# Kernel optimization log

Measured on AMD Instinct MI355X. Metric: run time of the kernel, lower is better.

Reference implementation:

```python
import jax, jax.numpy as jnp
import numpy as np
import math

B, S, D_MODEL = 2, 2048, 1024
H = 16
DK = D_MODEL // H          # 64, down-proj per-stream dim
NOPE, ROPE = 128, 64
D_HEAD = NOPE + ROPE       # 192 = d_latent // H
D_LATENT = H * D_HEAD      # 3072
ROT_DIM = 2 * ((ROPE // 2) // 2)  # rotary dim actually rotated = qk_rope_dim//2 = 32
EPS = 1e-6


def _rmsnorm(x, w):
    out = x * jax.lax.rsqrt(jnp.mean(x * x, axis=-1, keepdims=True) + EPS)
    return out * w


def _apply_rope(x):
    # x: [b, h, s, d]; rotate first ROT_DIM channels, interleaved pairing
    s = x.shape[-2]
    inv_freq = 1.0 / (10000.0 ** (jnp.arange(0, ROT_DIM, 2, dtype=jnp.float32) / ROT_DIM))
    freqs = jnp.arange(s, dtype=jnp.float32)[:, None] * inv_freq[None, :]  # [s, ROT_DIM//2]
    freqs = jnp.repeat(freqs, 2, axis=-1)  # [s, ROT_DIM], (f0,f0,f1,f1,...)
    cos, sin = jnp.cos(freqs), jnp.sin(freqs)
    xl, xr = x[..., :ROT_DIM], x[..., ROT_DIM:]
    x1, x2 = xl[..., 0::2], xl[..., 1::2]
    rot = jnp.stack([-x2, x1], axis=-1).reshape(xl.shape)
    xl = xl * cos + rot * sin
    return jnp.concatenate([xl, xr], axis=-1)


def setup_inputs() -> dict:
    key = jax.random.key(0)
    ks = jax.random.split(key, 5)
    sc = 0.02
    x = jax.random.normal(ks[0], (B, S, D_MODEL), jnp.float32)
    mask = jnp.broadcast_to(jnp.tril(jnp.ones((S, S), jnp.int32)), (B, S, S))
    w_down = jax.random.normal(ks[1], (D_MODEL, 3 * DK), jnp.float32) * sc
    rms_w = jnp.ones((3 * DK,), jnp.float32)
    w_up = jax.random.normal(ks[2], (3 * DK, 3 * D_LATENT), jnp.float32) * sc
    w_o = jax.random.normal(ks[3], (D_LATENT, D_MODEL), jnp.float32) * sc
    return {"x": x, "mask": mask, "w_down": w_down, "rms_w": rms_w, "w_up": w_up, "w_o": w_o}


def reference(x, mask, w_down, rms_w, w_up, w_o):
    h = x @ w_down                        # [b, s, 3*dk]
    h = _rmsnorm(h, rms_w)
    qkv = h @ w_up                        # [b, s, 3*d_latent]
    q, k, v = jnp.split(qkv, 3, axis=-1)  # each [b, s, d_latent]

    def to_heads(t):
        # einops '(d h)': d outer, h inner
        return t.reshape(B, S, D_HEAD, H).transpose(0, 3, 1, 2)  # [b, h, s, d]

    q, k, v = to_heads(q), to_heads(k), to_heads(v)
    q_nope, q_rope = q[..., :NOPE], q[..., NOPE:]
    k_nope, k_rope = k[..., :NOPE], k[..., NOPE:]
    q_rope = _apply_rope(q_rope)
    k_rope = _apply_rope(k_rope)

    scores = (jnp.einsum('bhid,bhjd->bhij', q_nope, k_nope)
              + jnp.einsum('bhid,bhjd->bhij', q_rope, k_rope))
    scores = scores / math.sqrt(NOPE + ROPE)
    scores = jnp.where(mask[:, None] == 0, -1e9, scores)
    attn = jax.nn.softmax(scores, axis=-1)

    out = jnp.einsum('bhij,bhjd->bhid', attn, v)        # [b, h, s, d]
    out = out.transpose(0, 2, 1, 3).reshape(B, S, D_LATENT)  # 'b h s d -> b s (h d)'
    return out @ w_o
```

## Files before the change

### kernel.cpp

```cpp
#include <hip/hip_runtime.h>
#include <stdint.h>
#include <stddef.h>


typedef __bf16 bf16x8 __attribute__((ext_vector_type(8)));
typedef float  f32x4  __attribute__((ext_vector_type(4)));

#define MFMA16x16(a,b,c) __builtin_amdgcn_mfma_f32_16x16x32_bf16((a),(b),(c),0,0,0)

__device__ __forceinline__ uint16_t f2bf(float f){
  union { float f; uint32_t u; } v; v.f = f;
  uint32_t u = v.u + 0x7fffu + ((v.u >> 16) & 1u);
  return (uint16_t)(u >> 16);
}
__device__ __forceinline__ bf16x8 load_frag(const uint16_t* p){
  uint4 u = *reinterpret_cast<const uint4*>(p);
  return __builtin_bit_cast(bf16x8, u);
}
__device__ __forceinline__ f32x4 fzero(){
  f32x4 z = {0.f, 0.f, 0.f, 0.f};
  return z;
}
__device__ __forceinline__ uint32_t pack2(float a, float b){
  return (uint32_t)f2bf(a) | ((uint32_t)f2bf(b) << 16);
}
__device__ __forceinline__ void gl2lds16(const uint16_t* g, uint16_t* l){
  __builtin_amdgcn_global_load_lds(
      (const __attribute__((address_space(1))) uint32_t*)g,
      (__attribute__((address_space(3))) uint32_t*)l,
      16, 0, 0);
}

__global__ __launch_bounds__(256) void k_transpose_all(const float* __restrict__ w_up,
                                                       const float* __restrict__ w_o,
                                                       const float* __restrict__ w_down,
                                                       uint16_t* __restrict__ w_up_t,
                                                       uint16_t* __restrict__ w_o_t,
                                                       uint16_t* __restrict__ w_dn_t){
  __shared__ float t[32][33];
  int id = blockIdx.x;
  const float* in; uint16_t* out; int R, C, bx, by;
  if(id < 1728){ in = w_up;  out = w_up_t; R = 192;  C = 9216; bx = id % 288; by = id / 288; }
  else if(id < 4800){ id -= 1728; in = w_o; out = w_o_t; R = 3072; C = 1024; bx = id % 32; by = id / 32; }
  else { id -= 4800; in = w_down; out = w_dn_t; R = 1024; C = 192; bx = id % 6; by = id / 6; }
  const int tc = bx * 32, tr = by * 32;
  const int j = threadIdx.x & 31, i0 = threadIdx.x >> 5;
  for(int ii = 0; ii < 4; ++ii){
    int r = i0 + ii * 8;
    t[r][j] = in[(size_t)(tr + r) * C + tc + j];
  }
  __syncthreads();
  for(int ii = 0; ii < 4; ++ii){
    int c = i0 + ii * 8;
    out[(size_t)(tc + c) * R + tr + j] = f2bf(t[j][c]);
  }
}

__global__ __launch_bounds__(256) void k_down_mfma(const float* __restrict__ x,
                                                   const uint16_t* __restrict__ wdt,
                                                   const float* __restrict__ rms_w,
                                                   uint16_t* __restrict__ h_out){
  __shared__ __align__(16) uint16_t as[32 * 64];
  __shared__ float hsq[32];
  const int tid  = threadIdx.x;
  const int wave = tid >> 6, lane = tid & 63;
  const int ml = lane & 15, qd = lane >> 4;
  const int m0 = blockIdx.x * 32;
  const int n0w = wave * 48;
  if(tid < 32) hsq[tid] = 0.f;

  f32x4 acc[2][3];
#pragma unroll
  for(int mt = 0; mt < 2; ++mt)
#pragma unroll
    for(int nt = 0; nt < 3; ++nt) acc[mt][nt] = fzero();

  const int srow = tid >> 3, sc = tid & 7;
  for(int kt = 0; kt < 16; ++kt){
    const float* src = x + (size_t)(m0 + srow) * 1024 + kt * 64 + sc * 8;
    float4 a = *reinterpret_cast<const float4*>(src);
    float4 b = *reinterpret_cast<const float4*>(src + 4);
    uint4 pk;
    pk.x = pack2(a.x, a.y); pk.y = pack2(a.z, a.w);
    pk.z = pack2(b.x, b.y); pk.w = pack2(b.z, b.w);
    __syncthreads();
    *reinterpret_cast<uint4*>(as + srow * 64 + ((sc ^ (srow & 7)) * 8)) = pk;
    __syncthreads();
#pragma unroll
    for(int kk = 0; kk < 2; ++kk){
      bf16x8 af[2];
#pragma unroll
      for(int mt = 0; mt < 2; ++mt){
        int row = mt * 16 + ml;
        af[mt] = load_frag(as + row * 64 + (((kk * 4 + qd) ^ (row & 7)) * 8));
      }
#pragma unroll
      for(int nt = 0; nt < 3; ++nt){
        bf16x8 bfr = load_frag(wdt + (size_t)(n0w + nt * 16 + ml) * 1024 + kt * 64 + kk * 32 + qd * 8);
#pragma unroll
        for(int mt = 0; mt < 2; ++mt)
          acc[mt][nt] = MFMA16x16(af[mt], bfr, acc[mt][nt]);
      }
    }
  }
  __syncthreads();
#pragma unroll
  for(int mt = 0; mt < 2; ++mt)
#pragma unroll
    for(int r = 0; r < 4; ++r){
      float s = acc[mt][0][r]*acc[mt][0][r] + acc[mt][1][r]*acc[mt][1][r] + acc[mt][2][r]*acc[mt][2][r];
#pragma unroll
      for(int off = 1; off < 16; off <<= 1) s += __shfl_xor(s, off);
      if(ml == 0) atomicAdd(&hsq[mt * 16 + qd * 4 + r], s);
    }
  __syncthreads();
  float rw[3];
#pragma unroll
  for(int nt = 0; nt < 3; ++nt) rw[nt] = rms_w[n0w + nt * 16 + ml];
#pragma unroll
  for(int mt = 0; mt < 2; ++mt)
#pragma unroll
    for(int r = 0; r < 4; ++r){
      int row = mt * 16 + qd * 4 + r;
      float scl = rsqrtf(hsq[row] * (1.0f / 192.0f) + 1e-6f);
#pragma unroll
      for(int nt = 0; nt < 3; ++nt)
        h_out[(size_t)(m0 + row) * 192 + n0w + nt * 16 + ml] = f2bf(acc[mt][nt][r] * scl * rw[nt]);
    }
}

__global__ __launch_bounds__(256) void k_gemm_up(const uint16_t* __restrict__ hmat,
                                                 const uint16_t* __restrict__ wt,
                                                 uint16_t* __restrict__ q_t,
                                                 uint16_t* __restrict__ k_t,
                                                 uint16_t* __restrict__ v_t){
  __shared__ __align__(16) uint16_t rp[16 * 129 * 8];
  const int wave = threadIdx.x >> 6, lane = threadIdx.x & 63;
  const int ml = lane & 15, qd = lane >> 4;
  const int m0 = blockIdx.y * 32;
  const int bx = blockIdx.x;
  const int which = bx / 6;
  const int d0b = (bx % 6) * 32;
  const int n0w = bx * 512 + wave * 128;
  const int d0w = d0b + wave * 8;

  bf16x8 af[2][6];
#pragma unroll
  for(int mt = 0; mt < 2; ++mt)
#pragma unroll
    for(int kk = 0; kk < 6; ++kk)
      af[mt][kk] = load_frag(hmat + (size_t)(m0 + mt * 16 + ml) * 192 + kk * 32 + qd * 8);

  f32x4 acc[8][2];
#pragma unroll
  for(int nt = 0; nt < 8; ++nt){ acc[nt][0] = fzero(); acc[nt][1] = fzero(); }
#pragma unroll
  for(int nt = 0; nt < 8; ++nt){
#pragma unroll
    for(int kk = 0; kk < 6; ++kk){
      bf16x8 b = load_frag(wt + (size_t)(n0w + nt * 16 + ml) * 192 + kk * 32 + qd * 8);
      acc[nt][0] = MFMA16x16(af[0][kk], b, acc[nt][0]);
      acc[nt][1] = MFMA16x16(af[1][kk], b, acc[nt][1]);
    }
  }

  const int b   = m0 >> 11;
  const int s0  = m0 & 2047;
  const int kt2 = s0 >> 6;
  const int row0 = s0 & 63;
  uint4* rp4 = (uint4*)rp;

  if(which < 2){
    const float qs = which ? 1.0f : 0.07216878364870322f;
    const bool rope = (d0w >= 128) && (d0w < 160);
#pragma unroll
    for(int mt = 0; mt < 2; ++mt)
#pragma unroll
      for(int r = 0; r < 4; ++r){
        int t = mt * 16 + qd * 4 + r;
        int s = s0 + t;
        float v[8];
#pragma unroll
        for(int nt = 0; nt < 8; ++nt) v[nt] = acc[nt][mt][r] * qs;
        if(rope){
#pragma unroll
          for(int pi = 0; pi < 4; ++pi){
            int fi = (d0w + 2 * pi - 128) >> 1;
            float invf = __expf(-(float)fi * 0.5756462732485114f);
            float sn, cs;
            sincosf((float)s * invf, &sn, &cs);
            float e = v[2 * pi], o = v[2 * pi + 1];
            v[2 * pi]     = e * cs - o * sn;
            v[2 * pi + 1] = o * cs + e * sn;
          }
        }
        uint4 pk;
        pk.x = pack2(v[0], v[1]); pk.y = pack2(v[2], v[3]);
        pk.z = pack2(v[4], v[5]); pk.w = pack2(v[6], v[7]);
        rp4[ml * 129 + t * 4 + (wave ^ (t & 3))] = pk;
      }
  } else {
#pragma unroll
    for(int nt = 0; nt < 8; ++nt){
      int dl = wave * 8 + nt;
#pragma unroll
      for(int mt = 0; mt < 2; ++mt){
        int jc = mt * 2 + (qd >> 1);
        int slot = ml * 129 + dl * 4 + (jc ^ (dl & 3));
        uint2 pk;
        pk.x = pack2(acc[nt][mt][0], acc[nt][mt][1]);
        pk.y = pack2(acc[nt][mt][2], acc[nt][mt][3]);
        *(reinterpret_cast<uint2*>(rp + slot * 8) + (qd & 1)) = pk;
      }
    }
  }
  __syncthreads();

  if(which < 2){
    uint16_t* dst = which ? k_t : q_t;
    const int cb = d0b >> 3;
#pragma unroll
    for(int it = 0; it < 8; ++it){
      int h = wave * 4 + (it & 3), rhalf = it >> 2;
      int tloc = rhalf * 16 + (lane >> 2), p = lane & 3;
      int row = row0 + tloc;
      uint4 val = rp4[h * 129 + tloc * 4 + p];
      size_t off = ((size_t)(b * 16 + h) * 32 + kt2) * 12288
                 + (size_t)row * 192 + ((cb ^ (tloc & 4)) + p) * 8;
      *reinterpret_cast<uint4*>(dst + off) = val;
    }
  } else {
    const int cs0 = row0 >> 3;
#pragma unroll
    for(int it = 0; it < 8; ++it){
      int h = wave * 4 + (it & 3), dhalf = it >> 2;
      int dl = dhalf * 16 + (lane >> 2), p = lane & 3;
      uint4 val = rp4[h * 129 + dl * 4 + p];
      size_t off = ((size_t)(b * 16 + h) * 32 + kt2) * 12288
                 + (size_t)(d0b + dl) * 64 + ((cs0 ^ (dl & 4)) + p) * 8;
      *reinterpret_cast<uint4*>(v_t + off) = val;
    }
  }
}

__global__ __launch_bounds__(256, 2) void k_attn(const uint16_t* __restrict__ q_t,
                                                 const uint16_t* __restrict__ k_t,
                                                 const uint16_t* __restrict__ v_t,
                                                 uint16_t* __restrict__ attn_out){
  __shared__ __align__(16) uint16_t lds[33792];
  uint16_t* ks = lds;
  uint16_t* vs = lds + 12288;
  uint16_t* ps = lds + 25600;
  const int tid  = threadIdx.x;
  const int wave = tid >> 6;
  const int lane = tid & 63;
  const int ml   = lane & 15;
  const int qd   = lane >> 4;
  const int L    = blockIdx.x;
  const int idx  = L >> 3;
  const int qt2  = 15 - (idx & 15);
  const int bh   = (L & 7) + ((idx >> 4) << 3);
  const int q0   = qt2 * 128;
  const int last = 2 * qt2 + 1;

  {
    uint32_t* vw = (uint32_t*)(lds + 24576);
    vw[tid] = 0x3F803F80u;
    vw[tid + 256] = 0x3F803F80u;
  }
  {
    const uint16_t* qsrc = q_t + ((size_t)bh * 32 + 2 * qt2) * 12288;
#pragma unroll
    for(int it = 0; it < 12; ++it){
      int seg = it * 4 + wave;
      gl2lds16(qsrc + seg * 512 + lane * 8, lds + seg * 512);
    }
  }
  __syncthreads();
  bf16x8 qf[2][6];
#pragma unroll
  for(int mg = 0; mg < 2; ++mg){
    int row = wave * 32 + mg * 16 + ml;
    int t64 = row >> 6, rl = row & 63;
#pragma unroll
    for(int kk = 0; kk < 6; ++kk)
      qf[mg][kk] = load_frag(lds + t64 * 12288 + rl * 192 + (((kk * 4 + qd) ^ (rl & 7)) * 8));
  }

  f32x4 o[2][13];
#pragma unroll
  for(int mg = 0; mg < 2; ++mg)
#pragma unroll
    for(int i = 0; i < 13; ++i) o[mg][i] = fzero();

  for(int kt = 0; kt <= last; ++kt){
    __syncthreads();
    const uint16_t* ktile = k_t + ((size_t)bh * 32 + kt) * 12288;
    const uint16_t* vtile = v_t + ((size_t)bh * 32 + kt) * 12288;
#pragma unroll
    for(int it = 0; it < 6; ++it){
      int seg = it * 4 + wave;
      gl2lds16(ktile + seg * 512 + lane * 8, ks + seg * 512);
      gl2lds16(vtile + seg * 512 + lane * 8, vs + seg * 512);
    }
    __syncthreads();

    const bool full_skip = (kt == last) && (wave < 2);
    if(!full_skip){
      const bool need_mask = (wave < 2) ? (kt == last - 1) : (kt == last);
#pragma unroll
      for(int mg = 0; mg < 2; ++mg){
        float p[4][4];
#pragma unroll
        for(int nt = 0; nt < 4; ++nt){
          f32x4 a = fzero();
          int row = nt * 16 + ml;
#pragma unroll
          for(int kk = 0; kk < 6; ++kk){
            bf16x8 bfr = load_frag(ks + row * 192 + (((kk * 4 + qd) ^ (row & 7)) * 8));
            a = MFMA16x16(qf[mg][kk], bfr, a);
          }
#pragma unroll
          for(int r = 0; r < 4; ++r){
            float e = __expf(a[r]);
            if(need_mask){
              int i = q0 + wave * 32 + mg * 16 + qd * 4 + r;
              int j = kt * 64 + nt * 16 + ml;
              if(j > i) e = 0.f;
            }
            p[nt][r] = e;
          }
        }
        uint16_t* psw = ps + wave * 2048 + mg * 1024;
#pragma unroll
        for(int nt = 0; nt < 4; ++nt)
#pragma unroll
          for(int r = 0; r < 4; ++r){
            int rp2 = qd * 4 + r;
            int col = nt * 16 + ml;
            int c = (col >> 3) ^ (rp2 & 7);
            psw[rp2 * 64 + c * 8 + (col & 7)] = f2bf(p[nt][r]);
          }
      }
#pragma unroll
      for(int kk2 = 0; kk2 < 2; ++kk2){
        int cp = (kk2 * 4 + qd) ^ (ml & 7);
        bf16x8 pa0 = load_frag(ps + wave * 2048 + ml * 64 + cp * 8);
        bf16x8 pa1 = load_frag(ps + wave * 2048 + 1024 + ml * 64 + cp * 8);
#pragma unroll
        for(int dt = 0; dt < 13; ++dt){
          int row = dt * 16 + ml;
          int cv = (kk2 * 4 + qd) ^ (row & 7);
          bf16x8 vb = load_frag(vs + row * 64 + cv * 8);
          o[0][dt] = MFMA16x16(pa0, vb, o[0][dt]);
          o[1][dt] = MFMA16x16(pa1, vb, o[1][dt]);
        }
      }
    }
  }

  const int hh = bh & 15, b = bh >> 4;
#pragma unroll
  for(int mg = 0; mg < 2; ++mg)
#pragma unroll
    for(int r = 0; r < 4; ++r){
      int i = q0 + wave * 32 + mg * 16 + qd * 4 + r;
      float inv = 1.0f / o[mg][12][r];
      size_t obase = ((size_t)b * 2048 + i) * 3072 + hh * 192;
#pragma unroll
      for(int dt = 0; dt < 12; ++dt)
        attn_out[obase + dt * 16 + ml] = f2bf(o[mg][dt][r] * inv);
    }
}

__global__ __launch_bounds__(256) void k_gemm_o_tile(const uint16_t* __restrict__ a,
                                                     const uint16_t* __restrict__ wt,
                                                     float* __restrict__ part){
  __shared__ __align__(16) uint16_t as[128 * 64];
  __shared__ __align__(16) uint16_t bs[128 * 64];
  const int wave = threadIdx.x >> 6, lane = threadIdx.x & 63;
  const int ml = lane & 15, qd = lane >> 4;
  const int m0 = blockIdx.y * 128, n0 = blockIdx.x * 128;
  const int kz = blockIdx.z;
  const int mo = (wave >> 1) * 64, no = (wave & 1) * 64;

  const int lrow = lane >> 3;
  const int gch  = (lane & 7) ^ (lrow & 7);
  const uint16_t* abase = a  + (size_t)(m0 + lrow) * 3072 + kz * 1536 + gch * 8;
  const uint16_t* bbase = wt + (size_t)(n0 + lrow) * 3072 + kz * 1536 + gch * 8;

  f32x4 acc[4][4];
#pragma unroll
  for(int mt = 0; mt < 4; ++mt)
#pragma unroll
    for(int nt = 0; nt < 4; ++nt) acc[mt][nt] = fzero();

  for(int kt = 0; kt < 24; ++kt){
    __syncthreads();
#pragma unroll
    for(int it = 0; it < 4; ++it){
      int seg = it * 4 + wave;
      gl2lds16(abase + (size_t)seg * 24576 + kt * 64, as + seg * 512);
      gl2lds16(bbase + (size_t)seg * 24576 + kt * 64, bs + seg * 512);
    }
    __syncthreads();
#pragma unroll
    for(int ks2 = 0; ks2 < 2; ++ks2){
      bf16x8 af[4], bfr[4];
#pragma unroll
      for(int mt = 0; mt < 4; ++mt){
        int row = mo + mt * 16 + ml;
        af[mt] = load_frag(as + row * 64 + (((ks2 * 4 + qd) ^ (row & 7)) * 8));
      }
#pragma unroll
      for(int nt = 0; nt < 4; ++nt){
        int row = no + nt * 16 + ml;
        bfr[nt] = load_frag(bs + row * 64 + (((ks2 * 4 + qd) ^ (row & 7)) * 8));
      }
#pragma unroll
      for(int mt = 0; mt < 4; ++mt)
#pragma unroll
        for(int nt = 0; nt < 4; ++nt)
          acc[mt][nt] = MFMA16x16(af[mt], bfr[nt], acc[mt][nt]);
    }
  }

  float* dst = part + (size_t)kz * 4096 * 1024;
#pragma unroll
  for(int mt = 0; mt < 4; ++mt)
#pragma unroll
    for(int nt = 0; nt < 4; ++nt)
#pragma unroll
      for(int r = 0; r < 4; ++r){
        int row = m0 + mo + mt * 16 + qd * 4 + r;
        int col = n0 + no + nt * 16 + ml;
        dst[(size_t)row * 1024 + col] = acc[mt][nt][r];
      }
}

__global__ __launch_bounds__(256) void k_addout(const float* __restrict__ part,
                                                float* __restrict__ out){
  int i = blockIdx.x * 256 + threadIdx.x;
  const float4* p0 = (const float4*)part;
  const float4* p1 = p0 + (size_t)1048576;
  float4 a = p0[i], b = p1[i];
  float4 c; c.x = a.x + b.x; c.y = a.y + b.y; c.z = a.z + b.z; c.w = a.w + b.w;
  ((float4*)out)[i] = c;
}


extern "C" void kernel_launch(void* const* d_in, const int* in_sizes, int n_in,
                              void* d_out, int out_size, void* d_ws, size_t ws_size,
                              hipStream_t stream) {
  (void)in_sizes; (void)n_in; (void)out_size; (void)ws_size;
  const float* x      = (const float*)d_in[0];
  const float* w_down = (const float*)d_in[2];
  const float* rms_w  = (const float*)d_in[3];
  const float* w_up   = (const float*)d_in[4];
  const float* w_o    = (const float*)d_in[5];
  float* out = (float*)d_out;

  char* ws = (char*)d_ws;
  uint16_t* h_bf   = (uint16_t*)(ws);
  uint16_t* w_up_t = (uint16_t*)(ws + 1572864);
  uint16_t* w_o_t  = (uint16_t*)(ws + 5111808);
  uint16_t* w_dn_t = (uint16_t*)(ws + 11403264);
  uint16_t* q_tb   = (uint16_t*)(ws + 11796480);
  uint16_t* k_tb   = (uint16_t*)(ws + 36962304);
  uint16_t* v_tb   = (uint16_t*)(ws + 62128128);
  uint16_t* attnO  = (uint16_t*)(ws + 87293952);
  float*    part   = (float*)(ws + 11796480);

  k_transpose_all<<<4992, 256, 0, stream>>>(w_up, w_o, w_down, w_up_t, w_o_t, w_dn_t);
  k_down_mfma<<<128, 256, 0, stream>>>(x, w_dn_t, rms_w, h_bf);
  k_gemm_up<<<dim3(18, 128), 256, 0, stream>>>(h_bf, w_up_t, q_tb, k_tb, v_tb);
  k_attn<<<512, 256, 0, stream>>>(q_tb, k_tb, v_tb, attnO);
  k_gemm_o_tile<<<dim3(8, 32, 2), 256, 0, stream>>>(attnO, w_o_t, part);
  k_addout<<<4096, 256, 0, stream>>>(part, out);
}
```

Baseline: 379.8 us.

## Restructure attention kernel to 8 waves with 16 rows each and reuse K LDS for P

The attention kernel moves from 4 waves handling 32 query rows each to 8 waves handling 16 rows each. This halves the per-thread accumulator and Q-fragment registers and raises the launch bound to 512 threads with 4 blocks per CU. It drops the separate P buffer in shared memory by writing P into the K tile region after an added barrier, which shrinks LDS per block so more blocks fit. The block-to-(bh, q-tile) mapping is also changed to alternate ascending and descending tile order for causal load balance. The cost is an extra __syncthreads per key tile and less reuse of each V fragment, since it now feeds one MFMA instead of two.

```diff
diff --git a/kernel.cpp b/kernel.cpp
--- a/kernel.cpp
+++ b/kernel.cpp
@@ -243,14 +243,13 @@
   }
 }
 
-__global__ __launch_bounds__(256, 2) void k_attn(const uint16_t* __restrict__ q_t,
+__global__ __launch_bounds__(512, 4) void k_attn(const uint16_t* __restrict__ q_t,
                                                  const uint16_t* __restrict__ k_t,
                                                  const uint16_t* __restrict__ v_t,
                                                  uint16_t* __restrict__ attn_out){
-  __shared__ __align__(16) uint16_t lds[33792];
+  __shared__ __align__(16) uint16_t lds[25600];
   uint16_t* ks = lds;
   uint16_t* vs = lds + 12288;
-  uint16_t* ps = lds + 25600;
   const int tid  = threadIdx.x;
   const int wave = tid >> 6;
   const int lane = tid & 63;
@@ -258,102 +257,94 @@
   const int qd   = lane >> 4;
   const int L    = blockIdx.x;
   const int idx  = L >> 3;
-  const int qt2  = 15 - (idx & 15);
-  const int bh   = (L & 7) + ((idx >> 4) << 3);
+  const int qt2  = (idx & 32) ? (idx & 15) : (15 - (idx & 15));
+  const int bh   = (L & 7) + 8 * ((idx >> 4) & 1) + 16 * (idx >> 5);
   const int q0   = qt2 * 128;
   const int last = 2 * qt2 + 1;
 
-  {
-    uint32_t* vw = (uint32_t*)(lds + 24576);
-    vw[tid] = 0x3F803F80u;
-    vw[tid + 256] = 0x3F803F80u;
-  }
+  ((uint32_t*)(vs + 12288))[tid] = 0x3F803F80u;
+
   {
     const uint16_t* qsrc = q_t + ((size_t)bh * 32 + 2 * qt2) * 12288;
 #pragma unroll
-    for(int it = 0; it < 12; ++it){
-      int seg = it * 4 + wave;
+    for(int it = 0; it < 6; ++it){
+      int seg = it * 8 + wave;
       gl2lds16(qsrc + seg * 512 + lane * 8, lds + seg * 512);
     }
   }
   __syncthreads();
-  bf16x8 qf[2][6];
-#pragma unroll
-  for(int mg = 0; mg < 2; ++mg){
-    int row = wave * 32 + mg * 16 + ml;
+  bf16x8 qf[6];
+  {
+    int row = wave * 16 + ml;
     int t64 = row >> 6, rl = row & 63;
 #pragma unroll
     for(int kk = 0; kk < 6; ++kk)
-      qf[mg][kk] = load_frag(lds + t64 * 12288 + rl * 192 + (((kk * 4 + qd) ^ (rl & 7)) * 8));
-  }
-
-  f32x4 o[2][13];
-#pragma unroll
-  for(int mg = 0; mg < 2; ++mg)
-#pragma unroll
-    for(int i = 0; i < 13; ++i) o[mg][i] = fzero();
+      qf[kk] = load_frag(lds + t64 * 12288 + rl * 192 + (((kk * 4 + qd) ^ (rl & 7)) * 8));
+  }
+
+  f32x4 o[13];
+#pragma unroll
+  for(int i = 0; i < 13; ++i) o[i] = fzero();
 
   for(int kt = 0; kt <= last; ++kt){
     __syncthreads();
     const uint16_t* ktile = k_t + ((size_t)bh * 32 + kt) * 12288;
     const uint16_t* vtile = v_t + ((size_t)bh * 32 + kt) * 12288;
 #pragma unroll
-    for(int it = 0; it < 6; ++it){
-      int seg = it * 4 + wave;
+    for(int it = 0; it < 3; ++it){
+      int seg = it * 8 + wave;
       gl2lds16(ktile + seg * 512 + lane * 8, ks + seg * 512);
       gl2lds16(vtile + seg * 512 + lane * 8, vs + seg * 512);
     }
     __syncthreads();
 
-    const bool full_skip = (kt == last) && (wave < 2);
+    const bool full_skip = (kt == last) && (wave < 4);
+    float p[4][4];
     if(!full_skip){
-      const bool need_mask = (wave < 2) ? (kt == last - 1) : (kt == last);
-#pragma unroll
-      for(int mg = 0; mg < 2; ++mg){
-        float p[4][4];
-#pragma unroll
-        for(int nt = 0; nt < 4; ++nt){
-          f32x4 a = fzero();
-          int row = nt * 16 + ml;
-#pragma unroll
-          for(int kk = 0; kk < 6; ++kk){
-            bf16x8 bfr = load_frag(ks + row * 192 + (((kk * 4 + qd) ^ (row & 7)) * 8));
-            a = MFMA16x16(qf[mg][kk], bfr, a);
+      const bool need_mask = (wave < 4) ? (kt == last - 1) : (kt == last);
+#pragma unroll
+      for(int nt = 0; nt < 4; ++nt){
+        f32x4 a = fzero();
+        int row = nt * 16 + ml;
+#pragma unroll
+        for(int kk = 0; kk < 6; ++kk){
+          bf16x8 bfr = load_frag(ks + row * 192 + (((kk * 4 + qd) ^ (row & 7)) * 8));
+          a = MFMA16x16(qf[kk], bfr, a);
+        }
+#pragma unroll
+        for(int r = 0; r < 4; ++r){
+          float e = __expf(a[r]);
+          if(need_mask){
+            int i = q0 + wave * 16 + qd * 4 + r;
+            int j = kt * 64 + nt * 16 + ml;
+            if(j > i) e = 0.f;
           }
-#pragma unroll
-          for(int r = 0; r < 4; ++r){
-            float e = __expf(a[r]);
-            if(need_mask){
-              int i = q0 + wave * 32 + mg * 16 + qd * 4 + r;
-              int j = kt * 64 + nt * 16 + ml;
-              if(j > i) e = 0.f;
-            }
-            p[nt][r] = e;
-          }
+          p[nt][r] = e;
         }
-        uint16_t* psw = ps + wave * 2048 + mg * 1024;
-#pragma unroll
-        for(int nt = 0; nt < 4; ++nt)
-#pragma unroll
-          for(int r = 0; r < 4; ++r){
-            int rp2 = qd * 4 + r;
-            int col = nt * 16 + ml;
-            int c = (col >> 3) ^ (rp2 & 7);
-            psw[rp2 * 64 + c * 8 + (col & 7)] = f2bf(p[nt][r]);
-          }
-      }
+      }
+    }
+    __syncthreads();
+    if(!full_skip){
+      uint16_t* psw = ks + wave * 1024;
+#pragma unroll
+      for(int nt = 0; nt < 4; ++nt)
+#pragma unroll
+        for(int r = 0; r < 4; ++r){
+          int rp2 = qd * 4 + r;
+          int col = nt * 16 + ml;
+          int c = (col >> 3) ^ (rp2 & 7);
+          psw[rp2 * 64 + c * 8 + (col & 7)] = f2bf(p[nt][r]);
+        }
 #pragma unroll
       for(int kk2 = 0; kk2 < 2; ++kk2){
         int cp = (kk2 * 4 + qd) ^ (ml & 7);
-        bf16x8 pa0 = load_frag(ps + wave * 2048 + ml * 64 + cp * 8);
-        bf16x8 pa1 = load_frag(ps + wave * 2048 + 1024 + ml * 64 + cp * 8);
+        bf16x8 pa = load_frag(psw + ml * 64 + cp * 8);
 #pragma unroll
         for(int dt = 0; dt < 13; ++dt){
           int row = dt * 16 + ml;
           int cv = (kk2 * 4 + qd) ^ (row & 7);
           bf16x8 vb = load_frag(vs + row * 64 + cv * 8);
-          o[0][dt] = MFMA16x16(pa0, vb, o[0][dt]);
-          o[1][dt] = MFMA16x16(pa1, vb, o[1][dt]);
+          o[dt] = MFMA16x16(pa, vb, o[dt]);
         }
       }
     }
@@ -361,16 +352,14 @@
 
   const int hh = bh & 15, b = bh >> 4;
 #pragma unroll
-  for(int mg = 0; mg < 2; ++mg)
-#pragma unroll
-    for(int r = 0; r < 4; ++r){
-      int i = q0 + wave * 32 + mg * 16 + qd * 4 + r;
-      float inv = 1.0f / o[mg][12][r];
-      size_t obase = ((size_t)b * 2048 + i) * 3072 + hh * 192;
-#pragma unroll
-      for(int dt = 0; dt < 12; ++dt)
-        attn_out[obase + dt * 16 + ml] = f2bf(o[mg][dt][r] * inv);
-    }
+  for(int r = 0; r < 4; ++r){
+    int i = q0 + wave * 16 + qd * 4 + r;
+    float inv = 1.0f / o[12][r];
+    size_t obase = ((size_t)b * 2048 + i) * 3072 + hh * 192;
+#pragma unroll
+    for(int dt = 0; dt < 12; ++dt)
+      attn_out[obase + dt * 16 + ml] = f2bf(o[dt][r] * inv);
+  }
 }
 
 __global__ __launch_bounds__(256) void k_gemm_o_tile(const uint16_t* __restrict__ a,
@@ -474,7 +463,7 @@
   k_transpose_all<<<4992, 256, 0, stream>>>(w_up, w_o, w_down, w_up_t, w_o_t, w_dn_t);
   k_down_mfma<<<128, 256, 0, stream>>>(x, w_dn_t, rms_w, h_bf);
   k_gemm_up<<<dim3(18, 128), 256, 0, stream>>>(h_bf, w_up_t, q_tb, k_tb, v_tb);
-  k_attn<<<512, 256, 0, stream>>>(q_tb, k_tb, v_tb, attnO);
+  k_attn<<<512, 512, 0, stream>>>(q_tb, k_tb, v_tb, attnO);
   k_gemm_o_tile<<<dim3(8, 32, 2), 256, 0, stream>>>(attnO, w_o_t, part);
   k_addout<<<4096, 256, 0, stream>>>(part, out);
 }
```

Result: no change. 382.2 us (+0.6%).
